# Kernel tuning notes

Hardware: AMD Instinct MI355X
Metric: run time of the kernel (lower is better)

## Reference

```python
import jax, jax.numpy as jnp
import numpy as np

B, C_IN, W, H = 16, 512, 40, 40
HC = 64  # hide_channel


def setup_inputs() -> dict:
    key = jax.random.key(0)
    ks = jax.random.split(key, 6)
    def xavier(k, shape):
        fan_in, fan_out = shape
        lim = np.sqrt(6.0 / (fan_in + fan_out))
        return jax.random.uniform(k, shape, jnp.float32, -lim, lim)
    return {
        "rgb": jax.random.normal(ks[0], (B, C_IN, W, H), jnp.float32),
        "hsi": jax.random.normal(ks[1], (B, C_IN, W, H), jnp.float32),
        "wq": xavier(ks[2], (C_IN, HC)),
        "wk": xavier(ks[3], (C_IN, HC)),
        "wv": xavier(ks[4], (C_IN, HC)),
        "wo": xavier(ks[5], (HC, C_IN)),
    }


def reference(rgb, hsi, wq, wk, wv, wo):
    b, c, w, h = rgb.shape
    n = w * h
    # [B, C, W, H] -> [B, N, C] tokens
    x0 = jnp.swapaxes(rgb.reshape(b, c, n), 1, 2)
    x1 = jnp.swapaxes(hsi.reshape(b, c, n), 1, 2)
    q = x0 @ wq              # [B, N, HC]
    k = x0 @ wk              # [B, N, HC]
    v = x1 @ wv              # [B, N, HC]
    hc = q.shape[-1]
    scale = hc ** (-0.5)
    attn = jax.nn.softmax(jnp.einsum('bnd,bmd->bnm', q, k) * scale, axis=-1)  # [B, N, N]
    res = jnp.einsum('bnm,bmd->bnd', attn, v)  # [B, N, HC]
    # Faithful to torch: .transpose(1, 2).reshape(B, N, HC) (layout reinterpretation)
    res = jnp.swapaxes(res, 1, 2).reshape(b, n, hc)
    out = res @ wo                              # [B, N, C]
    out = jnp.swapaxes(out, 1, 2).reshape(b, c, w, h)
    return out
```

## Files before the change

kernel.cpp:

```cpp
#include <hip/hip_runtime.h>
#include <cstddef>

#define NB   16
#define CIN  512
#define NTOK 1600
#define HCH  64
#define LDA  72

typedef __attribute__((ext_vector_type(8))) short bf16x8;
typedef __attribute__((ext_vector_type(4))) float f32x4;

__device__ __forceinline__ unsigned short f2bf(float x) {
    union { float f; unsigned u; } v; v.f = x;
    unsigned r = v.u + 0x7FFFu + ((v.u >> 16) & 1u);
    return (unsigned short)(r >> 16);
}

__global__ void __launch_bounds__(256) wprep_kernel(
    const float* __restrict__ wq, const float* __restrict__ wk,
    const float* __restrict__ wv, const float* __restrict__ wo,
    unsigned short* __restrict__ Wt, unsigned short* __restrict__ WoT)
{
    const int gid = blockIdx.x * 256 + threadIdx.x;
    if (gid < 3 * HCH * (CIN / 8)) {
        const int h  = gid & 63;
        const int c8 = (gid >> 6) & 63;
        const int t  = gid >> 12;
        const float* w = (t == 0) ? wq : (t == 1) ? wk : wv;
        ushort4 lo, hi;
        lo.x = f2bf(w[(size_t)(c8 * 8 + 0) * HCH + h]);
        lo.y = f2bf(w[(size_t)(c8 * 8 + 1) * HCH + h]);
        lo.z = f2bf(w[(size_t)(c8 * 8 + 2) * HCH + h]);
        lo.w = f2bf(w[(size_t)(c8 * 8 + 3) * HCH + h]);
        hi.x = f2bf(w[(size_t)(c8 * 8 + 4) * HCH + h]);
        hi.y = f2bf(w[(size_t)(c8 * 8 + 5) * HCH + h]);
        hi.z = f2bf(w[(size_t)(c8 * 8 + 6) * HCH + h]);
        hi.w = f2bf(w[(size_t)(c8 * 8 + 7) * HCH + h]);
        ushort4* dst = (ushort4*)(Wt + ((size_t)t * HCH + h) * CIN + c8 * 8);
        dst[0] = lo; dst[1] = hi;
    } else {
        const int g  = gid - 3 * HCH * (CIN / 8);
        const int c  = g & 511;
        const int j8 = g >> 9;
        ushort4 lo, hi;
        lo.x = f2bf(wo[(size_t)(j8 * 8 + 0) * CIN + c]);
        lo.y = f2bf(wo[(size_t)(j8 * 8 + 1) * CIN + c]);
        lo.z = f2bf(wo[(size_t)(j8 * 8 + 2) * CIN + c]);
        lo.w = f2bf(wo[(size_t)(j8 * 8 + 3) * CIN + c]);
        hi.x = f2bf(wo[(size_t)(j8 * 8 + 4) * CIN + c]);
        hi.y = f2bf(wo[(size_t)(j8 * 8 + 5) * CIN + c]);
        hi.z = f2bf(wo[(size_t)(j8 * 8 + 6) * CIN + c]);
        hi.w = f2bf(wo[(size_t)(j8 * 8 + 7) * CIN + c]);
        ushort4* dst = (ushort4*)(WoT + (size_t)c * HCH + j8 * 8);
        dst[0] = lo; dst[1] = hi;
    }
}

__global__ void __launch_bounds__(256) proj_kernel(
    const float* __restrict__ rgb, const float* __restrict__ hsi,
    const unsigned short* __restrict__ Wt,
    unsigned short* __restrict__ Q, unsigned short* __restrict__ K,
    unsigned short* __restrict__ Vt)
{
    __shared__ __align__(16) unsigned short As[64 * LDA];
    __shared__ __align__(16) unsigned short Ws[128 * LDA];

    const int which = blockIdx.y;
    const int b    = blockIdx.x / 25;
    const int n0   = (blockIdx.x % 25) * 64;
    const int tid  = threadIdx.x;
    const int wv_  = tid >> 6;
    const int lane = tid & 63;
    const int l16  = lane & 15, quad = lane >> 4;

    const float* __restrict__ src = which ? hsi : rgb;
    const unsigned short* __restrict__ wbase = Wt + (which ? (size_t)2 * HCH * CIN : 0);
    const int nW = which ? 1 : 2;

    f32x4 acc[2][4];
    #pragma unroll
    for (int t = 0; t < 2; ++t)
        #pragma unroll
        for (int nt = 0; nt < 4; ++nt)
            #pragma unroll
            for (int r = 0; r < 4; ++r) acc[t][nt][r] = 0.f;

    const int cc = tid >> 2;
    const int nq = tid & 3;

    for (int c0 = 0; c0 < CIN; c0 += 64) {
        __syncthreads();
        {
            const float* gs = src + ((size_t)b * CIN + c0 + cc) * NTOK + n0;
            #pragma unroll
            for (int rep = 0; rep < 4; ++rep) {
                const int nn4 = rep * 4 + nq;
                const float4 a = ((const float4*)gs)[nn4];
                const int n = nn4 * 4;
                As[(n + 0) * LDA + cc] = f2bf(a.x);
                As[(n + 1) * LDA + cc] = f2bf(a.y);
                As[(n + 2) * LDA + cc] = f2bf(a.z);
                As[(n + 3) * LDA + cc] = f2bf(a.w);
            }
        }
        for (int task = tid; task < nW * 512; task += 256) {
            const int row = task >> 3, ch = task & 7;
            *((int4*)(Ws + row * LDA + ch * 8)) =
                *((const int4*)(wbase + (size_t)row * CIN + c0 + ch * 8));
        }
        __syncthreads();

        #pragma unroll
        for (int k0 = 0; k0 < 2; ++k0) {
            const bf16x8 av = *((const bf16x8*)(As + (wv_ * 16 + l16) * LDA + k0 * 32 + quad * 8));
            if (which == 0) {
                #pragma unroll
                for (int t = 0; t < 2; ++t)
                    #pragma unroll
                    for (int nt = 0; nt < 4; ++nt) {
                        const bf16x8 bv = *((const bf16x8*)(Ws + (t * 64 + nt * 16 + l16) * LDA + k0 * 32 + quad * 8));
                        acc[t][nt] = __builtin_amdgcn_mfma_f32_16x16x32_bf16(av, bv, acc[t][nt], 0, 0, 0);
                    }
            } else {
                #pragma unroll
                for (int nt = 0; nt < 4; ++nt) {
                    const bf16x8 bv = *((const bf16x8*)(Ws + (nt * 16 + l16) * LDA + k0 * 32 + quad * 8));
                    acc[0][nt] = __builtin_amdgcn_mfma_f32_16x16x32_bf16(av, bv, acc[0][nt], 0, 0, 0);
                }
            }
        }
    }

    if (which == 0) {
        const float qscale = 0.18033688f;
        #pragma unroll
        for (int nt = 0; nt < 4; ++nt) {
            const int h = nt * 16 + l16;
            #pragma unroll
            for (int r = 0; r < 4; ++r) {
                const int n = n0 + wv_ * 16 + quad * 4 + r;
                Q[((size_t)b * NTOK + n) * HCH + h] = f2bf(acc[0][nt][r] * qscale);
                K[((size_t)b * NTOK + n) * HCH + h] = f2bf(acc[1][nt][r]);
            }
        }
    } else {
        #pragma unroll
        for (int nt = 0; nt < 4; ++nt) {
            const int h = nt * 16 + l16;
            ushort4 pv;
            pv.x = f2bf(acc[0][nt][0]); pv.y = f2bf(acc[0][nt][1]);
            pv.z = f2bf(acc[0][nt][2]); pv.w = f2bf(acc[0][nt][3]);
            *((ushort4*)(Vt + ((size_t)b * HCH + h) * NTOK + n0 + wv_ * 16 + quad * 4)) = pv;
        }
    }
}

__global__ void __launch_bounds__(256) attn_kernel(
    const unsigned short* __restrict__ Q, const unsigned short* __restrict__ K,
    const unsigned short* __restrict__ Vt, unsigned short* __restrict__ Rt2)
{
    __shared__ __align__(16) unsigned char smem[4 * 2 * 32 * LDA * 2];

    const int b    = blockIdx.x & 15;
    const int qt   = blockIdx.x >> 4;
    const int q0   = qt * 32;
    const int tid  = threadIdx.x;
    const int wv_  = tid >> 6;
    const int lane = tid & 63;
    const int l16  = lane & 15, quad = lane >> 4;

    const unsigned short* Qg = Q  + ((size_t)b * NTOK + q0) * HCH;
    const unsigned short* Kg = K  + (size_t)b * NTOK * HCH;
    const unsigned short* Vg = Vt + (size_t)b * HCH * NTOK;

    unsigned short* PsW = (unsigned short*)smem + wv_ * (2 * 32 * LDA);

    bf16x8 qa[2][2];
    #pragma unroll
    for (int qh = 0; qh < 2; ++qh)
        #pragma unroll
        for (int k0 = 0; k0 < 2; ++k0)
            qa[qh][k0] = *((const bf16x8*)(Qg + (size_t)(qh * 16 + l16) * HCH + k0 * 32 + quad * 8));

    f32x4 o[2][4];
    float rs[2][4];
    #pragma unroll
    for (int qh = 0; qh < 2; ++qh) {
        #pragma unroll
        for (int r = 0; r < 4; ++r) rs[qh][r] = 0.f;
        #pragma unroll
        for (int nt = 0; nt < 4; ++nt)
            #pragma unroll
            for (int r = 0; r < 4; ++r) o[qh][nt][r] = 0.f;
    }

    int buf = 0;
    for (int kt = wv_; kt < 25; kt += 4, buf ^= 1) {
        unsigned short* Pb = PsW + buf * (32 * LDA);

        bf16x8 kb[2][4], vb[2][4];
        #pragma unroll
        for (int k0 = 0; k0 < 2; ++k0)
            #pragma unroll
            for (int nt = 0; nt < 4; ++nt) {
                kb[k0][nt] = *((const bf16x8*)(Kg + ((size_t)(kt * 64 + nt * 16 + l16)) * HCH + k0 * 32 + quad * 8));
                vb[k0][nt] = *((const bf16x8*)(Vg + ((size_t)(nt * 16 + l16)) * NTOK + kt * 64 + k0 * 32 + quad * 8));
            }

        f32x4 s[2][4];
        #pragma unroll
        for (int qh = 0; qh < 2; ++qh)
            #pragma unroll
            for (int nt = 0; nt < 4; ++nt)
                #pragma unroll
                for (int r = 0; r < 4; ++r) s[qh][nt][r] = 0.f;
        #pragma unroll
        for (int k0 = 0; k0 < 2; ++k0)
            #pragma unroll
            for (int qh = 0; qh < 2; ++qh)
                #pragma unroll
                for (int nt = 0; nt < 4; ++nt)
                    s[qh][nt] = __builtin_amdgcn_mfma_f32_16x16x32_bf16(qa[qh][k0], kb[k0][nt], s[qh][nt], 0, 0, 0);

        #pragma unroll
        for (int qh = 0; qh < 2; ++qh)
            #pragma unroll
            for (int r = 0; r < 4; ++r) {
                #pragma unroll
                for (int nt = 0; nt < 4; ++nt) {
                    const float e = exp2f(s[qh][nt][r]);
                    rs[qh][r] += e;
                    Pb[(qh * 16 + quad * 4 + r) * LDA + nt * 16 + l16] = f2bf(e);
                }
            }

        #pragma unroll
        for (int k0 = 0; k0 < 2; ++k0)
            #pragma unroll
            for (int qh = 0; qh < 2; ++qh) {
                const bf16x8 pa = *((const bf16x8*)(Pb + (qh * 16 + l16) * LDA + k0 * 32 + quad * 8));
                #pragma unroll
                for (int nt = 0; nt < 4; ++nt)
                    o[qh][nt] = __builtin_amdgcn_mfma_f32_16x16x32_bf16(pa, vb[k0][nt], o[qh][nt], 0, 0, 0);
            }
    }

    #pragma unroll
    for (int qh = 0; qh < 2; ++qh)
        #pragma unroll
        for (int r = 0; r < 4; ++r)
            #pragma unroll
            for (int msk = 1; msk < 16; msk <<= 1)
                rs[qh][r] += __shfl_xor(rs[qh][r], msk, 16);

    __syncthreads();
    float* Osh = (float*)smem;
    float* lsh = (float*)(smem + 4 * 32 * 68 * 4);
    #pragma unroll
    for (int qh = 0; qh < 2; ++qh) {
        #pragma unroll
        for (int nt = 0; nt < 4; ++nt)
            #pragma unroll
            for (int r = 0; r < 4; ++r)
                Osh[(size_t)(wv_ * 32 + qh * 16 + quad * 4 + r) * 68 + nt * 16 + l16] = o[qh][nt][r];
        if (l16 == 0)
            #pragma unroll
            for (int r = 0; r < 4; ++r)
                lsh[wv_ * 32 + qh * 16 + quad * 4 + r] = rs[qh][r];
    }
    __syncthreads();

    const int t  = qt >> 1;
    const int jb = (qt & 1) * 32;
    const int h  = wv_ * 16 + l16;
    unsigned short* Rg = Rt2 + ((size_t)(b * 25 + t) * HCH + h) * HCH + jb;
    #pragma unroll
    for (int qh = 0; qh < 2; ++qh) {
        ushort4 pk;
        unsigned short pkv[4];
        #pragma unroll
        for (int r = 0; r < 4; ++r) {
            const int q = qh * 16 + quad * 4 + r;
            float val = 0.f, L = 0.f;
            #pragma unroll
            for (int w = 0; w < 4; ++w) {
                val += Osh[(size_t)(w * 32 + q) * 68 + h];
                L   += lsh[w * 32 + q];
            }
            pkv[r] = f2bf(val / L);
        }
        pk.x = pkv[0]; pk.y = pkv[1]; pk.z = pkv[2]; pk.w = pkv[3];
        *((ushort4*)(Rg + qh * 16 + quad * 4)) = pk;
    }
}

__global__ void __launch_bounds__(256) outproj_kernel(
    const unsigned short* __restrict__ Rt2, const unsigned short* __restrict__ WoT,
    float* __restrict__ out)
{
    __shared__ __align__(16) unsigned short Aw[64 * LDA];

    const int b    = blockIdx.x;
    const int ct   = blockIdx.y;
    const int nt64 = blockIdx.z;
    const int tid  = threadIdx.x;
    const int wv_  = tid >> 6;
    const int lane = tid & 63;
    const int l16  = lane & 15, quad = lane >> 4;

    #pragma unroll
    for (int r = 0; r < 2; ++r) {
        const int task = tid + r * 256;
        const int row = task >> 3, ch = task & 7;
        *((int4*)(Aw + row * LDA + ch * 8)) =
            *((const int4*)(WoT + ((size_t)(ct * 64 + row)) * HCH + ch * 8));
    }
    __syncthreads();

    const int n = nt64 * 64 + wv_ * 16 + l16;
    const int h = n / 25, t = n % 25;
    const unsigned short* bsrc = Rt2 + ((size_t)(b * 25 + t) * HCH + h) * HCH;

    f32x4 acc[4];
    #pragma unroll
    for (int mt = 0; mt < 4; ++mt)
        #pragma unroll
        for (int r = 0; r < 4; ++r) acc[mt][r] = 0.f;

    #pragma unroll
    for (int k0 = 0; k0 < 2; ++k0) {
        const bf16x8 bv = *((const bf16x8*)(bsrc + k0 * 32 + quad * 8));
        #pragma unroll
        for (int mt = 0; mt < 4; ++mt) {
            const bf16x8 av = *((const bf16x8*)(Aw + (mt * 16 + l16) * LDA + k0 * 32 + quad * 8));
            acc[mt] = __builtin_amdgcn_mfma_f32_16x16x32_bf16(av, bv, acc[mt], 0, 0, 0);
        }
    }
    #pragma unroll
    for (int mt = 0; mt < 4; ++mt)
        #pragma unroll
        for (int r = 0; r < 4; ++r)
            out[((size_t)b * CIN + ct * 64 + mt * 16 + quad * 4 + r) * NTOK + n] = acc[mt][r];
}

extern "C" void kernel_launch(void* const* d_in, const int* in_sizes, int n_in,
                              void* d_out, int out_size, void* d_ws, size_t ws_size,
                              hipStream_t stream)
{
    const float* rgb = (const float*)d_in[0];
    const float* hsi = (const float*)d_in[1];
    const float* wq  = (const float*)d_in[2];
    const float* wk  = (const float*)d_in[3];
    const float* wv  = (const float*)d_in[4];
    const float* wo  = (const float*)d_in[5];
    float* out = (float*)d_out;

    unsigned short* Wt  = (unsigned short*)d_ws;
    unsigned short* WoT = Wt  + (size_t)3 * HCH * CIN;
    unsigned short* Qb  = WoT + (size_t)CIN * HCH;
    unsigned short* Kb  = Qb  + (size_t)NB * NTOK * HCH;
    unsigned short* Vtb = Kb  + (size_t)NB * NTOK * HCH;
    unsigned short* Rt2 = Vtb + (size_t)NB * NTOK * HCH;

    wprep_kernel<<<dim3(64), 256, 0, stream>>>(wq, wk, wv, wo, Wt, WoT);
    proj_kernel<<<dim3(NB * 25, 2), 256, 0, stream>>>(rgb, hsi, Wt, Qb, Kb, Vtb);
    attn_kernel<<<dim3(NB * 50), 256, 0, stream>>>(Qb, Kb, Vtb, Rt2);
    outproj_kernel<<<dim3(NB, 8, 25), 256, 0, stream>>>(Rt2, WoT, out);
}
```

Baseline: 212.4 us.

## Keep attention probabilities in registers via transposed S MFMA, swizzle LDS, permute V

The S=QK^T MFMA now takes K as the A operand, so each lane holds scores for one query and four keys. The exponentiated probabilities are packed to bf16 with v_cvt_pk_bf16_f32 and fed straight into the PV MFMA as register operands, which removes the per-tile LDS round trip for P. To make that register layout line up, V's token columns are permuted when V is written in the projection kernel. The change also uses the hardware exp2, simplifies the row-sum reduction, XOR-swizzles the LDS activation tile in the projection kernel to cut bank conflicts, and loads K/V fragments on the fly instead of prefetching them all.

```diff
diff --git a/kernel.cpp b/kernel.cpp
--- a/kernel.cpp
+++ b/kernel.cpp
@@ -14,6 +14,20 @@
     union { float f; unsigned u; } v; v.f = x;
     unsigned r = v.u + 0x7FFFu + ((v.u >> 16) & 1u);
     return (unsigned short)(r >> 16);
+}
+
+__device__ __forceinline__ unsigned cvtpk_bf16(float lo, float hi) {
+    unsigned r;
+    asm("v_cvt_pk_bf16_f32 %0, %1, %2" : "=v"(r) : "v"(lo), "v"(hi));
+    return r;
+}
+
+__device__ __forceinline__ float fast_exp2(float x) {
+#if __has_builtin(__builtin_amdgcn_exp2f)
+    return __builtin_amdgcn_exp2f(x);
+#else
+    return exp2f(x);
+#endif
 }
 
 __global__ void __launch_bounds__(256) wprep_kernel(
@@ -87,6 +101,9 @@
 
     const int cc = tid >> 2;
     const int nq = tid & 3;
+    const int swz = cc >> 3;
+    const int clo = cc & 7;
+    const int swzr = (l16 >> 1) & 6;
 
     for (int c0 = 0; c0 < CIN; c0 += 64) {
         __syncthreads();
@@ -97,10 +114,12 @@
                 const int nn4 = rep * 4 + nq;
                 const float4 a = ((const float4*)gs)[nn4];
                 const int n = nn4 * 4;
-                As[(n + 0) * LDA + cc] = f2bf(a.x);
-                As[(n + 1) * LDA + cc] = f2bf(a.y);
-                As[(n + 2) * LDA + cc] = f2bf(a.z);
-                As[(n + 3) * LDA + cc] = f2bf(a.w);
+                const int i01 = ((swz ^ ((n >> 1) & 6)) << 3) + clo;
+                const int i23 = ((swz ^ (((n + 2) >> 1) & 6)) << 3) + clo;
+                As[(n + 0) * LDA + i01] = f2bf(a.x);
+                As[(n + 1) * LDA + i01] = f2bf(a.y);
+                As[(n + 2) * LDA + i23] = f2bf(a.z);
+                As[(n + 3) * LDA + i23] = f2bf(a.w);
             }
         }
         for (int task = tid; task < nW * 512; task += 256) {
@@ -112,7 +131,7 @@
 
         #pragma unroll
         for (int k0 = 0; k0 < 2; ++k0) {
-            const bf16x8 av = *((const bf16x8*)(As + (wv_ * 16 + l16) * LDA + k0 * 32 + quad * 8));
+            const bf16x8 av = *((const bf16x8*)(As + (wv_ * 16 + l16) * LDA + ((k0 * 4 + quad) ^ swzr) * 8));
             if (which == 0) {
                 #pragma unroll
                 for (int t = 0; t < 2; ++t)
@@ -144,13 +163,14 @@
             }
         }
     } else {
+        const int pbase = n0 + (wv_ & 1) * 32 + quad * 8 + (wv_ >> 1) * 4;
         #pragma unroll
         for (int nt = 0; nt < 4; ++nt) {
             const int h = nt * 16 + l16;
             ushort4 pv;
             pv.x = f2bf(acc[0][nt][0]); pv.y = f2bf(acc[0][nt][1]);
             pv.z = f2bf(acc[0][nt][2]); pv.w = f2bf(acc[0][nt][3]);
-            *((ushort4*)(Vt + ((size_t)b * HCH + h) * NTOK + n0 + wv_ * 16 + quad * 4)) = pv;
+            *((ushort4*)(Vt + ((size_t)b * HCH + h) * NTOK + pbase)) = pv;
         }
     }
 }
@@ -159,7 +179,7 @@
     const unsigned short* __restrict__ Q, const unsigned short* __restrict__ K,
     const unsigned short* __restrict__ Vt, unsigned short* __restrict__ Rt2)
 {
-    __shared__ __align__(16) unsigned char smem[4 * 2 * 32 * LDA * 2];
+    __shared__ __align__(16) unsigned char smem[4 * 32 * 68 * 4 + 4 * 32 * 4];
 
     const int b    = blockIdx.x & 15;
     const int qt   = blockIdx.x >> 4;
@@ -173,8 +193,6 @@
     const unsigned short* Kg = K  + (size_t)b * NTOK * HCH;
     const unsigned short* Vg = Vt + (size_t)b * HCH * NTOK;
 
-    unsigned short* PsW = (unsigned short*)smem + wv_ * (2 * 32 * LDA);
-
     bf16x8 qa[2][2];
     #pragma unroll
     for (int qh = 0; qh < 2; ++qh)
@@ -183,30 +201,15 @@
             qa[qh][k0] = *((const bf16x8*)(Qg + (size_t)(qh * 16 + l16) * HCH + k0 * 32 + quad * 8));
 
     f32x4 o[2][4];
-    float rs[2][4];
-    #pragma unroll
-    for (int qh = 0; qh < 2; ++qh) {
-        #pragma unroll
-        for (int r = 0; r < 4; ++r) rs[qh][r] = 0.f;
+    float rs[2] = {0.f, 0.f};
+    #pragma unroll
+    for (int qh = 0; qh < 2; ++qh)
         #pragma unroll
         for (int nt = 0; nt < 4; ++nt)
             #pragma unroll
             for (int r = 0; r < 4; ++r) o[qh][nt][r] = 0.f;
-    }
-
-    int buf = 0;
-    for (int kt = wv_; kt < 25; kt += 4, buf ^= 1) {
-        unsigned short* Pb = PsW + buf * (32 * LDA);
-
-        bf16x8 kb[2][4], vb[2][4];
-        #pragma unroll
-        for (int k0 = 0; k0 < 2; ++k0)
-            #pragma unroll
-            for (int nt = 0; nt < 4; ++nt) {
-                kb[k0][nt] = *((const bf16x8*)(Kg + ((size_t)(kt * 64 + nt * 16 + l16)) * HCH + k0 * 32 + quad * 8));
-                vb[k0][nt] = *((const bf16x8*)(Vg + ((size_t)(nt * 16 + l16)) * NTOK + kt * 64 + k0 * 32 + quad * 8));
-            }
-
+
+    for (int kt = wv_; kt < 25; kt += 4) {
         f32x4 s[2][4];
         #pragma unroll
         for (int qh = 0; qh < 2; ++qh)
@@ -217,43 +220,51 @@
         #pragma unroll
         for (int k0 = 0; k0 < 2; ++k0)
             #pragma unroll
-            for (int qh = 0; qh < 2; ++qh)
-                #pragma unroll
-                for (int nt = 0; nt < 4; ++nt)
-                    s[qh][nt] = __builtin_amdgcn_mfma_f32_16x16x32_bf16(qa[qh][k0], kb[k0][nt], s[qh][nt], 0, 0, 0);
-
+            for (int nt = 0; nt < 4; ++nt) {
+                const bf16x8 kf = *((const bf16x8*)(Kg + ((size_t)(kt * 64 + nt * 16 + l16)) * HCH + k0 * 32 + quad * 8));
+                s[0][nt] = __builtin_amdgcn_mfma_f32_16x16x32_bf16(kf, qa[0][k0], s[0][nt], 0, 0, 0);
+                s[1][nt] = __builtin_amdgcn_mfma_f32_16x16x32_bf16(kf, qa[1][k0], s[1][nt], 0, 0, 0);
+            }
+
+        unsigned dA[2][4], dB[2][4];
         #pragma unroll
         for (int qh = 0; qh < 2; ++qh)
             #pragma unroll
-            for (int r = 0; r < 4; ++r) {
-                #pragma unroll
-                for (int nt = 0; nt < 4; ++nt) {
-                    const float e = exp2f(s[qh][nt][r]);
-                    rs[qh][r] += e;
-                    Pb[(qh * 16 + quad * 4 + r) * LDA + nt * 16 + l16] = f2bf(e);
-                }
-            }
-
-        #pragma unroll
-        for (int k0 = 0; k0 < 2; ++k0)
+            for (int nt = 0; nt < 4; ++nt) {
+                const float e0 = fast_exp2(s[qh][nt][0]);
+                const float e1 = fast_exp2(s[qh][nt][1]);
+                const float e2 = fast_exp2(s[qh][nt][2]);
+                const float e3 = fast_exp2(s[qh][nt][3]);
+                rs[qh] += (e0 + e1) + (e2 + e3);
+                dA[qh][nt] = cvtpk_bf16(e0, e1);
+                dB[qh][nt] = cvtpk_bf16(e2, e3);
+            }
+
+        #pragma unroll
+        for (int k0 = 0; k0 < 2; ++k0) {
+            union { bf16x8 v; unsigned u[4]; } pu[2];
             #pragma unroll
             for (int qh = 0; qh < 2; ++qh) {
-                const bf16x8 pa = *((const bf16x8*)(Pb + (qh * 16 + l16) * LDA + k0 * 32 + quad * 8));
-                #pragma unroll
-                for (int nt = 0; nt < 4; ++nt)
-                    o[qh][nt] = __builtin_amdgcn_mfma_f32_16x16x32_bf16(pa, vb[k0][nt], o[qh][nt], 0, 0, 0);
-            }
-    }
-
-    #pragma unroll
-    for (int qh = 0; qh < 2; ++qh)
-        #pragma unroll
-        for (int r = 0; r < 4; ++r)
-            #pragma unroll
-            for (int msk = 1; msk < 16; msk <<= 1)
-                rs[qh][r] += __shfl_xor(rs[qh][r], msk, 16);
-
-    __syncthreads();
+                pu[qh].u[0] = dA[qh][k0];
+                pu[qh].u[1] = dB[qh][k0];
+                pu[qh].u[2] = dA[qh][k0 + 2];
+                pu[qh].u[3] = dB[qh][k0 + 2];
+            }
+            #pragma unroll
+            for (int nt = 0; nt < 4; ++nt) {
+                const bf16x8 vf = *((const bf16x8*)(Vg + ((size_t)(nt * 16 + l16)) * NTOK + kt * 64 + k0 * 32 + quad * 8));
+                o[0][nt] = __builtin_amdgcn_mfma_f32_16x16x32_bf16(pu[0].v, vf, o[0][nt], 0, 0, 0);
+                o[1][nt] = __builtin_amdgcn_mfma_f32_16x16x32_bf16(pu[1].v, vf, o[1][nt], 0, 0, 0);
+            }
+        }
+    }
+
+    #pragma unroll
+    for (int qh = 0; qh < 2; ++qh) {
+        rs[qh] += __shfl_xor(rs[qh], 16);
+        rs[qh] += __shfl_xor(rs[qh], 32);
+    }
+
     float* Osh = (float*)smem;
     float* lsh = (float*)(smem + 4 * 32 * 68 * 4);
     #pragma unroll
@@ -263,10 +274,8 @@
             #pragma unroll
             for (int r = 0; r < 4; ++r)
                 Osh[(size_t)(wv_ * 32 + qh * 16 + quad * 4 + r) * 68 + nt * 16 + l16] = o[qh][nt][r];
-        if (l16 == 0)
-            #pragma unroll
-            for (int r = 0; r < 4; ++r)
-                lsh[wv_ * 32 + qh * 16 + quad * 4 + r] = rs[qh][r];
+        if (quad == 0)
+            lsh[wv_ * 32 + qh * 16 + l16] = rs[qh];
     }
     __syncthreads();
 
```

After: 218.7 us. +3.0%, slower.
